# Kernel optimization log

Hardware: AMD Instinct MI355X
Metric: run time of the kernel (lower is better)

Reference implementation:

```python
import jax, jax.numpy as jnp
import numpy as np

DIM = 768
NUM_HEADS = 12
HIDDEN = int(DIM * 4.0)
EPS = 1e-5


def setup_inputs() -> dict:
    key = jax.random.key(0)
    ks = jax.random.split(key, 8)
    s = lambda k, shape, scale=0.02: jax.random.normal(k, shape, dtype=jnp.float32) * scale
    return {
        "x": jax.random.normal(ks[0], (8, 1024, DIM), dtype=jnp.float32),
        "ln1_g": jnp.ones((DIM,), jnp.float32),
        "ln1_b": jnp.zeros((DIM,), jnp.float32),
        "qkv_w": s(ks[1], (DIM, 3 * DIM)),
        "qkv_b": jnp.zeros((3 * DIM,), jnp.float32),
        "proj_w": s(ks[2], (DIM, DIM)),
        "proj_b": jnp.zeros((DIM,), jnp.float32),
        "ln2_g": jnp.ones((DIM,), jnp.float32),
        "ln2_b": jnp.zeros((DIM,), jnp.float32),
        "fc1_w": s(ks[3], (DIM, HIDDEN)),
        "fc1_b": jnp.zeros((HIDDEN,), jnp.float32),
        "fc2_w": s(ks[4], (HIDDEN, DIM)),
        "fc2_b": jnp.zeros((DIM,), jnp.float32),
    }


def layer_norm(x, g, b):
    mu = jnp.mean(x, axis=-1, keepdims=True)
    var = jnp.mean(jnp.square(x - mu), axis=-1, keepdims=True)
    return (x - mu) * jax.lax.rsqrt(var + EPS) * g + b


def reference(x, ln1_g, ln1_b, qkv_w, qkv_b, proj_w, proj_b,
              ln2_g, ln2_b, fc1_w, fc1_b, fc2_w, fc2_b):
    B, N, C = x.shape
    H = NUM_HEADS
    Dh = C // H
    scale = Dh ** -0.5

    # --- Attention (pre-norm) ---
    h = layer_norm(x, ln1_g, ln1_b)
    qkv = h @ qkv_w + qkv_b                       # [B, N, 3C]
    qkv = qkv.reshape(B, N, 3, H, Dh)
    q, k, v = qkv[:, :, 0], qkv[:, :, 1], qkv[:, :, 2]  # [B, N, H, Dh]
    attn = jnp.einsum("bqhd,bkhd->bhqk", q, k) * scale  # [B, H, N, N]
    attn = jax.nn.softmax(attn, axis=-1)
    o = jnp.einsum("bhqk,bkhd->bqhd", attn, v).reshape(B, N, C)
    x = x + (o @ proj_w + proj_b)

    # --- MLP (pre-norm) ---
    h = layer_norm(x, ln2_g, ln2_b)
    h = jax.nn.gelu(h @ fc1_w + fc1_b, approximate=False)  # torch nn.GELU = exact erf
    x = x + (h @ fc2_w + fc2_b)
    return x
```

## Files before the change

### kernel.cpp

```cpp
#include <hip/hip_runtime.h>
#include <hip/hip_bf16.h>
#include <cstdint>

using f32x4  = __attribute__((ext_vector_type(4))) float;
using bf16x8 = __attribute__((ext_vector_type(8))) short;

__device__ inline ushort f2bf(float f) {
    union { float f; uint u; } x; x.f = f;
    uint u = x.u;
    return (ushort)((u + 0x7FFFu + ((u >> 16) & 1u)) >> 16);
}

__device__ inline void unpack8(uint4 v, float* out) {
    uint ws[4] = {v.x, v.y, v.z, v.w};
#pragma unroll
    for (int i = 0; i < 4; ++i) {
        union { uint u; float f; } lo, hi;
        lo.u = ws[i] << 16;
        hi.u = ws[i] & 0xFFFF0000u;
        out[2 * i]     = lo.f;
        out[2 * i + 1] = hi.f;
    }
}

__device__ inline void gload16(const ushort* g, ushort* lds) {
    __builtin_amdgcn_global_load_lds(
        (const __attribute__((address_space(1))) unsigned int*)g,
        (__attribute__((address_space(3))) unsigned int*)lds, 16, 0, 0);
}

__global__ __launch_bounds__(256) void transpose_cast(const float* __restrict__ w,
                                                      ushort* __restrict__ wt,
                                                      int K, int N) {
    __shared__ float tile[32][33];
    const int bn = blockIdx.x * 32;
    const int bk = blockIdx.y * 32;
    const int tx = threadIdx.x & 31, ty = threadIdx.x >> 5;
#pragma unroll
    for (int i = 0; i < 32; i += 8)
        tile[ty + i][tx] = w[(size_t)(bk + ty + i) * N + bn + tx];
    __syncthreads();
#pragma unroll
    for (int i = 0; i < 32; i += 8)
        wt[(size_t)(bn + ty + i) * K + bk + tx] = f2bf(tile[tx][ty + i]);
}

__global__ __launch_bounds__(256) void ln_bf16(const float* __restrict__ x,
                                               const float* __restrict__ g,
                                               const float* __restrict__ b,
                                               ushort* __restrict__ out) {
    const int row = blockIdx.x;
    const float* xr = x + (size_t)row * 768;
    const int t = threadIdx.x;
    float v0 = xr[t], v1 = xr[t + 256], v2 = xr[t + 512];
    float s  = v0 + v1 + v2;
    float sq = v0 * v0 + v1 * v1 + v2 * v2;
#pragma unroll
    for (int off = 32; off > 0; off >>= 1) {
        s  += __shfl_down(s, off);
        sq += __shfl_down(sq, off);
    }
    __shared__ float sa[4], sb[4];
    const int wv = t >> 6, lane = t & 63;
    if (lane == 0) { sa[wv] = s; sb[wv] = sq; }
    __syncthreads();
    s  = sa[0] + sa[1] + sa[2] + sa[3];
    sq = sb[0] + sb[1] + sb[2] + sb[3];
    const float mu   = s * (1.0f / 768.0f);
    const float var  = sq * (1.0f / 768.0f) - mu * mu;
    const float rstd = rsqrtf(var + 1e-5f);
    ushort* orow = out + (size_t)row * 768;
    orow[t]       = f2bf((v0 - mu) * rstd * g[t]       + b[t]);
    orow[t + 256] = f2bf((v1 - mu) * rstd * g[t + 256] + b[t + 256]);
    orow[t + 512] = f2bf((v2 - mu) * rstd * g[t + 512] + b[t + 512]);
}

template <int EPI>
__global__ __launch_bounds__(256) void gemm_bt(const ushort* __restrict__ A,
                                               const ushort* __restrict__ Bt,
                                               const float* __restrict__ bias,
                                               const float* __restrict__ resid,
                                               void* __restrict__ out,
                                               void* __restrict__ out2,
                                               int M, int N, int K) {
    __shared__ ushort As[2][128 * 32];
    __shared__ ushort Bs[2][128 * 32];
    const int bm   = blockIdx.y * 128, bn = blockIdx.x * 128;
    const int t    = threadIdx.x;
    const int lane = t & 63;
    const int w    = t >> 6;
    const int wr   = w >> 1, wc = w & 1;
    const int lr   = lane >> 4, lc = lane & 15;

    const f32x4 fzero = {0.f, 0.f, 0.f, 0.f};
    f32x4 acc[4][4];
#pragma unroll
    for (int ai = 0; ai < 4; ++ai)
#pragma unroll
        for (int bj = 0; bj < 4; ++bj) acc[ai][bj] = fzero;

    const int srow = lane >> 2;
    const int sk8  = (lane & 3) * 8;
    const ushort* Ag0 = A  + (size_t)(bm + w * 16 + srow) * K + sk8;
    const ushort* Ag1 = Ag0 + (size_t)64 * K;
    const ushort* Bg0 = Bt + (size_t)(bn + w * 16 + srow) * K + sk8;
    const ushort* Bg1 = Bg0 + (size_t)64 * K;
    const int lo0 = (w * 16) * 32, lo1 = (64 + w * 16) * 32;

    const int nt = K >> 5;
    gload16(Ag0, &As[0][lo0]);
    gload16(Ag1, &As[0][lo1]);
    gload16(Bg0, &Bs[0][lo0]);
    gload16(Bg1, &Bs[0][lo1]);
    __syncthreads();

    int cur = 0;
    for (int tk = 0; tk < nt; ++tk) {
        if (tk + 1 < nt) {
            int kb = (tk + 1) << 5;
            gload16(Ag0 + kb, &As[cur ^ 1][lo0]);
            gload16(Ag1 + kb, &As[cur ^ 1][lo1]);
            gload16(Bg0 + kb, &Bs[cur ^ 1][lo0]);
            gload16(Bg1 + kb, &Bs[cur ^ 1][lo1]);
        }
        bf16x8 af[4], bf[4];
#pragma unroll
        for (int ai = 0; ai < 4; ++ai)
            af[ai] = *(const bf16x8*)&As[cur][(wr * 64 + ai * 16 + lc) * 32 + lr * 8];
#pragma unroll
        for (int bj = 0; bj < 4; ++bj)
            bf[bj] = *(const bf16x8*)&Bs[cur][(wc * 64 + bj * 16 + lc) * 32 + lr * 8];
#pragma unroll
        for (int ai = 0; ai < 4; ++ai)
#pragma unroll
            for (int bj = 0; bj < 4; ++bj)
                acc[ai][bj] = __builtin_amdgcn_mfma_f32_16x16x32_bf16(af[ai], bf[bj],
                                                                      acc[ai][bj], 0, 0, 0);
        __syncthreads();
        cur ^= 1;
    }

#pragma unroll
    for (int ai = 0; ai < 4; ++ai) {
#pragma unroll
        for (int bj = 0; bj < 4; ++bj) {
            int col  = bn + wc * 64 + bj * 16 + lc;
            float bs = bias[col];
            if (EPI == 3 && col >= 1536) {
                int row0 = bm + wr * 64 + ai * 16 + lr * 4;
                int bb   = row0 >> 10, key0 = row0 & 1023;
                int c    = col - 1536;
                int h    = c >> 6, d = c & 63;
                ushort4 pk;
                pk.x = f2bf(acc[ai][bj][0] + bs);
                pk.y = f2bf(acc[ai][bj][1] + bs);
                pk.z = f2bf(acc[ai][bj][2] + bs);
                pk.w = f2bf(acc[ai][bj][3] + bs);
                *(ushort4*)((ushort*)out2 +
                            ((size_t)(bb * 12 + h) * 64 + d) * 1024 + key0) = pk;
                continue;
            }
#pragma unroll
            for (int j = 0; j < 4; ++j) {
                int row   = bm + wr * 64 + ai * 16 + lr * 4 + j;
                float val = acc[ai][bj][j] + bs;
                if (EPI == 1) {
                    val += resid[(size_t)row * N + col];
                    ((float*)out)[(size_t)row * N + col] = val;
                } else if (EPI == 2) {
                    val = 0.5f * val * (1.0f + erff(val * 0.70710678118f));
                    ((ushort*)out)[(size_t)row * N + col] = f2bf(val);
                } else {
                    ((ushort*)out)[(size_t)row * N + col] = f2bf(val);
                }
            }
        }
    }
}

__global__ __launch_bounds__(256) void attn_mfma(const ushort* __restrict__ qkv,
                                                 const ushort* __restrict__ vT,
                                                 ushort* __restrict__ outb) {
    __shared__ ushort Kls[64 * 72];
    __shared__ ushort Vtls[64 * 72];
    __shared__ ushort Pls[4][32 * 72];

    const int bid = blockIdx.x;
    const int b   = bid / 96;
    const int rem = bid % 96;
    const int h   = rem >> 3;
    const int qc  = rem & 7;
    const int t    = threadIdx.x;
    const int w    = t >> 6;
    const int lane = t & 63;
    const int lr   = lane >> 4, lc = lane & 15;
    const int q0   = qc * 128 + w * 32;
    const size_t bbase = (size_t)b * 1024;
    const ushort* vTh = vT + ((size_t)(b * 12 + h) * 64) * 1024;

    bf16x8 qa[2][2];
#pragma unroll
    for (int rt = 0; rt < 2; ++rt)
#pragma unroll
        for (int ds = 0; ds < 2; ++ds) {
            uint4 u = *(const uint4*)(qkv + (bbase + q0 + rt * 16 + lc) * 2304 +
                                      h * 64 + ds * 32 + lr * 8);
            float tmp[8];
            unpack8(u, tmp);
            bf16x8 v;
#pragma unroll
            for (int j = 0; j < 8; ++j) v[j] = (short)f2bf(tmp[j] * 0.125f);
            qa[rt][ds] = v;
        }

    const f32x4 fzero = {0.f, 0.f, 0.f, 0.f};
    f32x4 O[2][4];
    float m[2][4], l[2][4];
#pragma unroll
    for (int rt = 0; rt < 2; ++rt) {
#pragma unroll
        for (int dt = 0; dt < 4; ++dt) O[rt][dt] = fzero;
#pragma unroll
        for (int j = 0; j < 4; ++j) { m[rt][j] = -INFINITY; l[rt][j] = 0.0f; }
    }

    for (int kt = 0; kt < 16; ++kt) {
        const int k0 = kt * 64;
        __syncthreads();
#pragma unroll
        for (int i = 0; i < 2; ++i) {
            int idx = t + i * 256;
            int key = idx >> 3, seg = idx & 7;
            uint4 u = *(const uint4*)(qkv + (bbase + k0 + key) * 2304 + 768 +
                                      h * 64 + seg * 8);
            *(uint4*)&Kls[key * 72 + seg * 8] = u;
        }
#pragma unroll
        for (int i = 0; i < 2; ++i) {
            int idx = t + i * 256;
            int d = idx >> 3, seg = idx & 7;
            uint4 u = *(const uint4*)(vTh + (size_t)d * 1024 + k0 + seg * 8);
            *(uint4*)&Vtls[d * 72 + seg * 8] = u;
        }
        __syncthreads();

        f32x4 s4[2][4];
#pragma unroll
        for (int rt = 0; rt < 2; ++rt)
#pragma unroll
            for (int kt4 = 0; kt4 < 4; ++kt4) {
                f32x4 acc = fzero;
#pragma unroll
                for (int ds = 0; ds < 2; ++ds) {
                    bf16x8 kb = *(const bf16x8*)&Kls[(kt4 * 16 + lc) * 72 + ds * 32 + lr * 8];
                    acc = __builtin_amdgcn_mfma_f32_16x16x32_bf16(qa[rt][ds], kb, acc, 0, 0, 0);
                }
                s4[rt][kt4] = acc;
            }

#pragma unroll
        for (int rt = 0; rt < 2; ++rt) {
#pragma unroll
            for (int j = 0; j < 4; ++j) {
                float v = fmaxf(fmaxf(s4[rt][0][j], s4[rt][1][j]),
                                fmaxf(s4[rt][2][j], s4[rt][3][j]));
#pragma unroll
                for (int off = 1; off < 16; off <<= 1) v = fmaxf(v, __shfl_xor(v, off));
                float mn = fmaxf(m[rt][j], v);
                float c  = __expf(m[rt][j] - mn);
                m[rt][j] = mn;
                float psum = 0.f;
#pragma unroll
                for (int kt4 = 0; kt4 < 4; ++kt4) {
                    float p = __expf(s4[rt][kt4][j] - mn);
                    s4[rt][kt4][j] = p;
                    psum += p;
                }
#pragma unroll
                for (int off = 1; off < 16; off <<= 1) psum += __shfl_xor(psum, off);
                l[rt][j] = l[rt][j] * c + psum;
#pragma unroll
                for (int dt = 0; dt < 4; ++dt) O[rt][dt][j] *= c;
                int prow = rt * 16 + lr * 4 + j;
#pragma unroll
                for (int kt4 = 0; kt4 < 4; ++kt4)
                    Pls[w][prow * 72 + kt4 * 16 + lc] = f2bf(s4[rt][kt4][j]);
            }
        }

        bf16x8 pa[2][2];
#pragma unroll
        for (int rt = 0; rt < 2; ++rt)
#pragma unroll
            for (int ks = 0; ks < 2; ++ks)
                pa[rt][ks] = *(const bf16x8*)&Pls[w][(rt * 16 + lc) * 72 + ks * 32 + lr * 8];
#pragma unroll
        for (int dt = 0; dt < 4; ++dt)
#pragma unroll
            for (int ks = 0; ks < 2; ++ks) {
                bf16x8 vb = *(const bf16x8*)&Vtls[(dt * 16 + lc) * 72 + ks * 32 + lr * 8];
#pragma unroll
                for (int rt = 0; rt < 2; ++rt)
                    O[rt][dt] = __builtin_amdgcn_mfma_f32_16x16x32_bf16(pa[rt][ks], vb,
                                                                        O[rt][dt], 0, 0, 0);
            }
    }

#pragma unroll
    for (int rt = 0; rt < 2; ++rt)
#pragma unroll
        for (int j = 0; j < 4; ++j) {
            float inv = 1.0f / l[rt][j];
            size_t row = bbase + q0 + rt * 16 + lr * 4 + j;
#pragma unroll
            for (int dt = 0; dt < 4; ++dt)
                outb[row * 768 + h * 64 + dt * 16 + lc] = f2bf(O[rt][dt][j] * inv);
        }
}

extern "C" void kernel_launch(void* const* d_in, const int* in_sizes, int n_in,
                              void* d_out, int out_size, void* d_ws, size_t ws_size,
                              hipStream_t stream) {
    const float* x      = (const float*)d_in[0];
    const float* ln1_g  = (const float*)d_in[1];
    const float* ln1_b  = (const float*)d_in[2];
    const float* qkv_w  = (const float*)d_in[3];
    const float* qkv_b  = (const float*)d_in[4];
    const float* proj_w = (const float*)d_in[5];
    const float* proj_b = (const float*)d_in[6];
    const float* ln2_g  = (const float*)d_in[7];
    const float* ln2_b  = (const float*)d_in[8];
    const float* fc1_w  = (const float*)d_in[9];
    const float* fc1_b  = (const float*)d_in[10];
    const float* fc2_w  = (const float*)d_in[11];
    const float* fc2_b  = (const float*)d_in[12];

    char* ws = (char*)d_ws;
    auto alloc = [&](size_t bytes) {
        char* p = ws;
        ws += (bytes + 255) & ~(size_t)255;
        return p;
    };
    ushort* qkv_wt  = (ushort*)alloc((size_t)768 * 2304 * 2);
    ushort* proj_wt = (ushort*)alloc((size_t)768 * 768 * 2);
    ushort* fc1_wt  = (ushort*)alloc((size_t)768 * 3072 * 2);
    ushort* fc2_wt  = (ushort*)alloc((size_t)3072 * 768 * 2);
    ushort* hb      = (ushort*)alloc((size_t)8192 * 768 * 2);
    ushort* qkvb    = (ushort*)alloc((size_t)8192 * 2304 * 2);
    ushort* vTb     = (ushort*)alloc((size_t)96 * 64 * 1024 * 2);
    ushort* ob      = (ushort*)alloc((size_t)8192 * 768 * 2);
    float*  x1      = (float*)alloc((size_t)8192 * 768 * 4);
    ushort* h2b     = (ushort*)alloc((size_t)8192 * 768 * 2);
    ushort* h3b     = (ushort*)alloc((size_t)8192 * 3072 * 2);

    transpose_cast<<<dim3(2304 / 32, 768 / 32), 256, 0, stream>>>(qkv_w, qkv_wt, 768, 2304);
    transpose_cast<<<dim3(768 / 32, 768 / 32), 256, 0, stream>>>(proj_w, proj_wt, 768, 768);
    transpose_cast<<<dim3(3072 / 32, 768 / 32), 256, 0, stream>>>(fc1_w, fc1_wt, 768, 3072);
    transpose_cast<<<dim3(768 / 32, 3072 / 32), 256, 0, stream>>>(fc2_w, fc2_wt, 3072, 768);

    ln_bf16<<<8192, 256, 0, stream>>>(x, ln1_g, ln1_b, hb);
    gemm_bt<3><<<dim3(2304 / 128, 8192 / 128), 256, 0, stream>>>(hb, qkv_wt, qkv_b, nullptr,
                                                                 qkvb, vTb, 8192, 2304, 768);
    attn_mfma<<<768, 256, 0, stream>>>(qkvb, vTb, ob);
    gemm_bt<1><<<dim3(768 / 128, 8192 / 128), 256, 0, stream>>>(ob, proj_wt, proj_b, x,
                                                                x1, nullptr, 8192, 768, 768);
    ln_bf16<<<8192, 256, 0, stream>>>(x1, ln2_g, ln2_b, h2b);
    gemm_bt<2><<<dim3(3072 / 128, 8192 / 128), 256, 0, stream>>>(h2b, fc1_wt, fc1_b, nullptr,
                                                                 h3b, nullptr, 8192, 3072, 768);
    gemm_bt<1><<<dim3(768 / 128, 8192 / 128), 256, 0, stream>>>(h3b, fc2_wt, fc2_b, x1,
                                                                (float*)d_out, nullptr,
                                                                8192, 768, 3072);
}
```

Baseline: 340.7 us.

## Rewrite attention with transposed 32x32x16 MFMA and register-resident P

The flash-attention kernel now computes S^T = K·Q^T and O^T = V^T·P^T with 32x32x16 bf16 MFMAs instead of 16x16x32 tiles. Each lane then owns one query row, so the softmax max and sum need only a single cross-half shuffle instead of 4-step butterflies. P is repacked in registers with lane-xor-32 shuffles instead of being staged through LDS, which removes the per-wave P shared buffer and its stores and loads. Output is written as packed 4-element stores. The risks are higher register pressure from the 16-wide accumulators and getting the operand layout of the transposed MFMAs right.

```diff
diff --git a/kernel.cpp b/kernel.cpp
--- a/kernel.cpp
+++ b/kernel.cpp
@@ -2,8 +2,9 @@
 #include <hip/hip_bf16.h>
 #include <cstdint>
 
-using f32x4  = __attribute__((ext_vector_type(4))) float;
-using bf16x8 = __attribute__((ext_vector_type(8))) short;
+using f32x4   = __attribute__((ext_vector_type(4))) float;
+using f32x16  = __attribute__((ext_vector_type(16))) float;
+using bf16x8  = __attribute__((ext_vector_type(8))) short;
 
 __device__ inline ushort f2bf(float f) {
     union { float f; uint u; } x; x.f = f;
@@ -183,7 +184,6 @@
                                                  ushort* __restrict__ outb) {
     __shared__ ushort Kls[64 * 72];
     __shared__ ushort Vtls[64 * 72];
-    __shared__ ushort Pls[4][32 * 72];
 
     const int bid = blockIdx.x;
     const int b   = bid / 96;
@@ -193,36 +193,33 @@
     const int t    = threadIdx.x;
     const int w    = t >> 6;
     const int lane = t & 63;
-    const int lr   = lane >> 4, lc = lane & 15;
+    const int l31  = lane & 31;
+    const int hi   = lane >> 5;
     const int q0   = qc * 128 + w * 32;
     const size_t bbase = (size_t)b * 1024;
     const ushort* vTh = vT + ((size_t)(b * 12 + h) * 64) * 1024;
 
-    bf16x8 qa[2][2];
-#pragma unroll
-    for (int rt = 0; rt < 2; ++rt)
-#pragma unroll
-        for (int ds = 0; ds < 2; ++ds) {
-            uint4 u = *(const uint4*)(qkv + (bbase + q0 + rt * 16 + lc) * 2304 +
-                                      h * 64 + ds * 32 + lr * 8);
+    bf16x8 qb[4];
+    {
+        const size_t qrow = (bbase + q0 + l31) * 2304 + h * 64;
+#pragma unroll
+        for (int dblk = 0; dblk < 4; ++dblk) {
+            uint4 u = *(const uint4*)(qkv + qrow + dblk * 16 + hi * 8);
             float tmp[8];
             unpack8(u, tmp);
             bf16x8 v;
 #pragma unroll
             for (int j = 0; j < 8; ++j) v[j] = (short)f2bf(tmp[j] * 0.125f);
-            qa[rt][ds] = v;
-        }
-
-    const f32x4 fzero = {0.f, 0.f, 0.f, 0.f};
-    f32x4 O[2][4];
-    float m[2][4], l[2][4];
-#pragma unroll
-    for (int rt = 0; rt < 2; ++rt) {
-#pragma unroll
-        for (int dt = 0; dt < 4; ++dt) O[rt][dt] = fzero;
-#pragma unroll
-        for (int j = 0; j < 4; ++j) { m[rt][j] = -INFINITY; l[rt][j] = 0.0f; }
-    }
+            qb[dblk] = v;
+        }
+    }
+
+    f32x16 O[2];
+#pragma unroll
+    for (int ob = 0; ob < 2; ++ob)
+#pragma unroll
+        for (int r = 0; r < 16; ++r) O[ob][r] = 0.0f;
+    float m = -INFINITY, l = 0.0f;
 
     for (int kt = 0; kt < 16; ++kt) {
         const int k0 = kt * 64;
@@ -244,77 +241,87 @@
         }
         __syncthreads();
 
-        f32x4 s4[2][4];
-#pragma unroll
-        for (int rt = 0; rt < 2; ++rt)
-#pragma unroll
-            for (int kt4 = 0; kt4 < 4; ++kt4) {
-                f32x4 acc = fzero;
-#pragma unroll
-                for (int ds = 0; ds < 2; ++ds) {
-                    bf16x8 kb = *(const bf16x8*)&Kls[(kt4 * 16 + lc) * 72 + ds * 32 + lr * 8];
-                    acc = __builtin_amdgcn_mfma_f32_16x16x32_bf16(qa[rt][ds], kb, acc, 0, 0, 0);
-                }
-                s4[rt][kt4] = acc;
-            }
-
-#pragma unroll
-        for (int rt = 0; rt < 2; ++rt) {
-#pragma unroll
-            for (int j = 0; j < 4; ++j) {
-                float v = fmaxf(fmaxf(s4[rt][0][j], s4[rt][1][j]),
-                                fmaxf(s4[rt][2][j], s4[rt][3][j]));
-#pragma unroll
-                for (int off = 1; off < 16; off <<= 1) v = fmaxf(v, __shfl_xor(v, off));
-                float mn = fmaxf(m[rt][j], v);
-                float c  = __expf(m[rt][j] - mn);
-                m[rt][j] = mn;
-                float psum = 0.f;
-#pragma unroll
-                for (int kt4 = 0; kt4 < 4; ++kt4) {
-                    float p = __expf(s4[rt][kt4][j] - mn);
-                    s4[rt][kt4][j] = p;
-                    psum += p;
-                }
-#pragma unroll
-                for (int off = 1; off < 16; off <<= 1) psum += __shfl_xor(psum, off);
-                l[rt][j] = l[rt][j] * c + psum;
-#pragma unroll
-                for (int dt = 0; dt < 4; ++dt) O[rt][dt][j] *= c;
-                int prow = rt * 16 + lr * 4 + j;
-#pragma unroll
-                for (int kt4 = 0; kt4 < 4; ++kt4)
-                    Pls[w][prow * 72 + kt4 * 16 + lc] = f2bf(s4[rt][kt4][j]);
-            }
-        }
-
-        bf16x8 pa[2][2];
-#pragma unroll
-        for (int rt = 0; rt < 2; ++rt)
-#pragma unroll
-            for (int ks = 0; ks < 2; ++ks)
-                pa[rt][ks] = *(const bf16x8*)&Pls[w][(rt * 16 + lc) * 72 + ks * 32 + lr * 8];
-#pragma unroll
-        for (int dt = 0; dt < 4; ++dt)
-#pragma unroll
-            for (int ks = 0; ks < 2; ++ks) {
-                bf16x8 vb = *(const bf16x8*)&Vtls[(dt * 16 + lc) * 72 + ks * 32 + lr * 8];
-#pragma unroll
-                for (int rt = 0; rt < 2; ++rt)
-                    O[rt][dt] = __builtin_amdgcn_mfma_f32_16x16x32_bf16(pa[rt][ks], vb,
-                                                                        O[rt][dt], 0, 0, 0);
-            }
-    }
-
-#pragma unroll
-    for (int rt = 0; rt < 2; ++rt)
-#pragma unroll
-        for (int j = 0; j < 4; ++j) {
-            float inv = 1.0f / l[rt][j];
-            size_t row = bbase + q0 + rt * 16 + lr * 4 + j;
-#pragma unroll
-            for (int dt = 0; dt < 4; ++dt)
-                outb[row * 768 + h * 64 + dt * 16 + lc] = f2bf(O[rt][dt][j] * inv);
+        f32x16 s[2];
+#pragma unroll
+        for (int kb = 0; kb < 2; ++kb) {
+            f32x16 acc;
+#pragma unroll
+            for (int r = 0; r < 16; ++r) acc[r] = 0.0f;
+#pragma unroll
+            for (int dblk = 0; dblk < 4; ++dblk) {
+                bf16x8 ka = *(const bf16x8*)&Kls[(kb * 32 + l31) * 72 + dblk * 16 + hi * 8];
+                acc = __builtin_amdgcn_mfma_f32_32x32x16_bf16(ka, qb[dblk], acc, 0, 0, 0);
+            }
+            s[kb] = acc;
+        }
+
+        float v = s[0][0];
+#pragma unroll
+        for (int r = 1; r < 16; ++r) v = fmaxf(v, s[0][r]);
+#pragma unroll
+        for (int r = 0; r < 16; ++r) v = fmaxf(v, s[1][r]);
+        v = fmaxf(v, __shfl_xor(v, 32));
+        float mn = fmaxf(m, v);
+        float c  = __expf(m - mn);
+        m = mn;
+        float psum = 0.0f;
+#pragma unroll
+        for (int kb = 0; kb < 2; ++kb)
+#pragma unroll
+            for (int r = 0; r < 16; ++r) {
+                float p = __expf(s[kb][r] - mn);
+                s[kb][r] = p;
+                psum += p;
+            }
+        psum += __shfl_xor(psum, 32);
+        l = l * c + psum;
+#pragma unroll
+        for (int ob = 0; ob < 2; ++ob)
+#pragma unroll
+            for (int r = 0; r < 16; ++r) O[ob][r] *= c;
+
+        bf16x8 pb[4];
+#pragma unroll
+        for (int kb16 = 0; kb16 < 4; ++kb16) {
+            const int sb = kb16 >> 1, r0 = (kb16 & 1) * 8;
+            uint own01 = (uint)f2bf(s[sb][r0 + 0]) | ((uint)f2bf(s[sb][r0 + 1]) << 16);
+            uint own23 = (uint)f2bf(s[sb][r0 + 2]) | ((uint)f2bf(s[sb][r0 + 3]) << 16);
+            uint own45 = (uint)f2bf(s[sb][r0 + 4]) | ((uint)f2bf(s[sb][r0 + 5]) << 16);
+            uint own67 = (uint)f2bf(s[sb][r0 + 6]) | ((uint)f2bf(s[sb][r0 + 7]) << 16);
+            uint sw01 = __shfl_xor(own01, 32);
+            uint sw23 = __shfl_xor(own23, 32);
+            uint sw45 = __shfl_xor(own45, 32);
+            uint sw67 = __shfl_xor(own67, 32);
+            uint d0 = hi ? sw45 : own01;
+            uint d1 = hi ? sw67 : own23;
+            uint d2 = hi ? own45 : sw01;
+            uint d3 = hi ? own67 : sw23;
+            union { uint u[4]; bf16x8 v; } cvt;
+            cvt.u[0] = d0; cvt.u[1] = d1; cvt.u[2] = d2; cvt.u[3] = d3;
+            pb[kb16] = cvt.v;
+        }
+
+#pragma unroll
+        for (int ob = 0; ob < 2; ++ob)
+#pragma unroll
+            for (int kb16 = 0; kb16 < 4; ++kb16) {
+                bf16x8 va = *(const bf16x8*)&Vtls[(ob * 32 + l31) * 72 + kb16 * 16 + hi * 8];
+                O[ob] = __builtin_amdgcn_mfma_f32_32x32x16_bf16(va, pb[kb16], O[ob], 0, 0, 0);
+            }
+    }
+
+    const float inv = 1.0f / l;
+    ushort* orow = outb + (bbase + q0 + l31) * 768 + h * 64;
+#pragma unroll
+    for (int ob = 0; ob < 2; ++ob)
+#pragma unroll
+        for (int qd = 0; qd < 4; ++qd) {
+            ushort4 pk;
+            pk.x = f2bf(O[ob][qd * 4 + 0] * inv);
+            pk.y = f2bf(O[ob][qd * 4 + 1] * inv);
+            pk.z = f2bf(O[ob][qd * 4 + 2] * inv);
+            pk.w = f2bf(O[ob][qd * 4 + 3] * inv);
+            *(ushort4*)(orow + ob * 32 + qd * 8 + hi * 4) = pk;
         }
 }
 
```

New measurement: 304.0 us. 10.8% less time.
